# Performance work log

Hardware: AMD Instinct MI355X
Metric: run time of the kernel (lower is better)

Reference implementation:

```python
import jax, jax.numpy as jnp
import numpy as np

N_TIME = 512          # n_time_nodes
LATENT = 32           # latent_dim
HIDDEN = 64           # hidden_dim
N_MODES = 8           # r_fourier_modes
X_A0 = 0.3            # initial stoichiometry (anode)
CSANMAX = 28700.0     # max concentration scale
BASE_LOGIT = float(np.log(X_A0 / (1.0 - X_A0)))  # logit_from_fraction(x_a0)
FEAT_DIM = 1 + 2 * N_MODES   # [rho, cos(k*pi*rho), sin(k*pi*rho)]
IN_DIM = LATENT + FEAT_DIM
N_POINTS = 2_000_000


def setup_inputs() -> dict:
    key = jax.random.key(0)
    ks = jax.random.split(key, 8)
    time_idx = jax.random.randint(ks[0], (N_POINTS,), 0, N_TIME)
    rho = jax.random.uniform(ks[1], (N_POINTS,), dtype=jnp.float32)
    # trainable latent code per nonzero time node
    emb = jax.random.normal(ks[2], (N_TIME - 1, LATENT), dtype=jnp.float32) * 0.02
    # decoder_a: Linear(IN,HID)+SiLU, Linear(HID,HID)+SiLU, Linear(HID,1)
    W0 = jax.random.normal(ks[3], (IN_DIM, HIDDEN), dtype=jnp.float32) / np.sqrt(IN_DIM)
    b0 = jnp.zeros((HIDDEN,), jnp.float32)
    W1 = jax.random.normal(ks[4], (HIDDEN, HIDDEN), dtype=jnp.float32) / np.sqrt(HIDDEN)
    b1 = jnp.zeros((HIDDEN,), jnp.float32)
    Wout = jax.random.normal(ks[5], (HIDDEN, 1), dtype=jnp.float32) * 0.1
    bout = jnp.zeros((1,), jnp.float32)
    return {"time_idx": time_idx, "rho": rho, "emb": emb,
            "W0": W0, "b0": b0, "W1": W1, "b1": b1, "Wout": Wout, "bout": bout}


def _radius_features(rho):
    # [N] -> [N, 1 + 2*N_MODES]
    k = jnp.arange(1, N_MODES + 1, dtype=rho.dtype)
    ang = jnp.pi * rho[:, None] * k[None, :]
    return jnp.concatenate([rho[:, None], jnp.cos(ang), jnp.sin(ang)], axis=1)


def reference(time_idx, rho, emb, W0, b0, W1, b1, Wout, bout):
    # predicated version of the torch masked scatter: compute everywhere,
    # select initial-condition value where time_idx == 0
    idx = jnp.clip(time_idx - 1, 0, N_TIME - 2)       # safe gather index
    e = emb[idx]                                       # [N, LATENT]
    feat = _radius_features(rho)                       # [N, FEAT_DIM]
    h = jnp.concatenate([e, feat], axis=1)             # [N, IN_DIM]
    h = jax.nn.silu(h @ W0 + b0)
    h = jax.nn.silu(h @ W1 + b1)
    raw = (h @ Wout + bout)[:, 0]                      # [N]
    theta = jax.nn.sigmoid(raw + BASE_LOGIT)
    return jnp.where(time_idx == 0, X_A0 * CSANMAX, theta * CSANMAX)
```

## Files before the change

kernel.cpp:

```cpp
#include <hip/hip_runtime.h>
#include <stdint.h>


typedef _Float16 half8  __attribute__((ext_vector_type(8)));
typedef _Float16 half4v __attribute__((ext_vector_type(4)));
typedef _Float16 half2v __attribute__((ext_vector_type(2)));
typedef float f32x4 __attribute__((ext_vector_type(4)));

#define LOG2E 1.44269504088896340736f
#define BASE_LOGIT -0.84729786038720367f
#define CSANMAX 28700.0f
#define IC_VAL 8610.0f

__device__ __forceinline__ float fast_exp2(float x) { return __builtin_amdgcn_exp2f(x); }
__device__ __forceinline__ float fast_rcp(float x)  { return __builtin_amdgcn_rcpf(x); }
__device__ __forceinline__ float sigf(float x)  { return fast_rcp(1.0f + fast_exp2(-LOG2E * x)); }
__device__ __forceinline__ void silu2(float x0, float x1, float& y0, float& y1) {
  const float d0 = 1.0f + fast_exp2(-LOG2E * x0);
  const float d1 = 1.0f + fast_exp2(-LOG2E * x1);
  const float r  = fast_rcp(d0 * d1);
  y0 = x0 * d1 * r;
  y1 = x1 * d0 * r;
}
__device__ __forceinline__ half2v pkh(float a, float b) {
  return __builtin_bit_cast(half2v, __builtin_amdgcn_cvt_pkrtz(a, b));
}

union H8 { half8 v8; half2v v2[4]; };
union H4 { half4v v4; half2v v2[2]; };

template <int CTRL>
__device__ __forceinline__ float dpp_radd(float x) {
  int yi = __builtin_amdgcn_update_dpp(0, __builtin_bit_cast(int, x), CTRL, 0xF, 0xF, false);
  return x + __builtin_bit_cast(float, yi);
}
__device__ __forceinline__ float row_sum16(float x) {
  x = dpp_radd<0xB1>(x);
  x = dpp_radd<0x4E>(x);
  x = dpp_radd<0x141>(x);
  x = dpp_radd<0x140>(x);
  return x;
}

__global__ __launch_bounds__(128) void mlp_kernel(
    const int* __restrict__ tix, const float* __restrict__ rho,
    const float* __restrict__ emb, const float* __restrict__ W0,
    const float* __restrict__ b0, const float* __restrict__ W1,
    const float* __restrict__ b1, const float* __restrict__ Wout,
    const float* __restrict__ bout, float* __restrict__ out, int ngroups)
{
  __shared__ __align__(16) _Float16 ldsF[2][64][40];
  __shared__ __align__(16) _Float16 ldsH[2][2][16][72];

  const int tid  = threadIdx.x;
  const int wid  = tid >> 6;
  const int lane = tid & 63;
  const int m    = lane & 15;
  const int q    = lane >> 4;

  _Float16 (*F)[40]      = ldsF[wid];
  _Float16 (*Hd)[16][72] = ldsH[wid];

  half8 B0f[4][2], B1f[4][2];
#pragma unroll
  for (int t = 0; t < 4; ++t) {
#pragma unroll
    for (int s = 0; s < 2; ++s) {
      half8 f0, f1;
#pragma unroll
      for (int j = 0; j < 8; ++j) {
        const int k = s * 32 + q * 8 + j;
        const int n = t * 16 + m;
        const float v0 = (k < 49) ? W0[k * 64 + n] : ((k == 49) ? b0[n] : 0.0f);
        f0[j] = (_Float16)v0;
        f1[j] = (_Float16)W1[k * 64 + n];
      }
      B0f[t][s] = f0;
      B1f[t][s] = f1;
    }
  }
  float b1n[4], woutm[4];
#pragma unroll
  for (int t = 0; t < 4; ++t) {
    b1n[t]   = b1[t * 16 + m];
    woutm[t] = Wout[t * 16 + m];
  }
  const float boutBL = bout[0] + BASE_LOGIT;

  {
    half8 zc = (half8)(_Float16)0.0f;
    *(half8*)&F[lane][16] = zc;
    *(half8*)&F[lane][24] = zc;
  }

  const f32x4 z = {0.0f, 0.0f, 0.0f, 0.0f};
  const int gwaves = gridDim.x * 2;

  int g = blockIdx.x * 2 + wid;
  if (g >= ngroups) return;

  int   tiL = tix[g * 64 + lane];
  float rh  = rho[g * 64 + lane];

  for (; g < ngroups; g += gwaves) {
    const int gbase = g * 64;

    const int gn = (g + gwaves < ngroups) ? (g + gwaves) : g;
    const int   tiLn = tix[gn * 64 + lane];
    const float rhn  = rho[gn * 64 + lane];

    int tim4[4];
#pragma unroll
    for (int st = 0; st < 4; ++st) tim4[st] = __shfl(tiL, st * 16 + m, 64);
    const float* erow0 = emb + (size_t)min(max(tim4[0] - 1, 0), 510) * 32 + q * 8;
    f32x4 eA0 = *(const f32x4*)erow0;
    f32x4 eA1 = *(const f32x4*)(erow0 + 4);

    const float rev = 0.5f * rh;
    const float c1 = __builtin_amdgcn_cosf(rev);
    const float s1 = __builtin_amdgcn_sinf(rev);
    float cs[8], sn[8];
    cs[0] = c1; sn[0] = s1;
    {
      float cm2 = 1.0f, cm1 = c1, sm2 = 0.0f, sm1 = s1;
      const float tc = 2.0f * c1;
#pragma unroll
      for (int k = 1; k < 8; ++k) {
        const float ck = tc * cm1 - cm2;
        const float sk = tc * sm1 - sm2;
        cs[k] = ck; sn[k] = sk;
        cm2 = cm1; cm1 = ck; sm2 = sm1; sm1 = sk;
      }
    }
    H8 h0, h1;
    h0.v2[0] = pkh(rh,    cs[0]); h0.v2[1] = pkh(cs[1], cs[2]);
    h0.v2[2] = pkh(cs[3], cs[4]); h0.v2[3] = pkh(cs[5], cs[6]);
    h1.v2[0] = pkh(cs[7], sn[0]); h1.v2[1] = pkh(sn[1], sn[2]);
    h1.v2[2] = pkh(sn[3], sn[4]); h1.v2[3] = pkh(sn[5], sn[6]);
    *(half8*)&F[lane][0] = h0.v8;
    *(half8*)&F[lane][8] = h1.v8;
    *(half2v*)&F[lane][16] = pkh(sn[7], 1.0f);

    float dcar = 0.0f;

#pragma unroll
    for (int st = 0; st < 4; ++st) {
      _Float16 (*Hb)[72] = Hd[st & 1];

      f32x4 eB0, eB1;
      if (st < 3) {
        const float* erown = emb + (size_t)min(max(tim4[st + 1] - 1, 0), 510) * 32 + q * 8;
        eB0 = *(const f32x4*)erown;
        eB1 = *(const f32x4*)(erown + 4);
      }

      H8 X0;
      X0.v2[0] = pkh(eA0[0], eA0[1]); X0.v2[1] = pkh(eA0[2], eA0[3]);
      X0.v2[2] = pkh(eA1[0], eA1[1]); X0.v2[3] = pkh(eA1[2], eA1[3]);
      const half8 X1 = *(const half8*)&F[st * 16 + m][q * 8];

      f32x4 acc[4];
#pragma unroll
      for (int t = 0; t < 4; ++t) {
        f32x4 a = __builtin_amdgcn_mfma_f32_16x16x32_f16(B0f[t][0], X0.v8, z, 0, 0, 0);
        a = __builtin_amdgcn_mfma_f32_16x16x32_f16(B0f[t][1], X1, a, 0, 0, 0);
        acc[t] = a;
      }
#pragma unroll
      for (int t = 0; t < 4; ++t) {
        float s0, s1v, s2, s3;
        silu2(acc[t][0], acc[t][1], s0, s1v);
        silu2(acc[t][2], acc[t][3], s2, s3);
        H4 hh;
        hh.v2[0] = pkh(s0, s1v);
        hh.v2[1] = pkh(s2, s3);
        *(half4v*)&Hb[m][t * 16 + q * 4] = hh.v4;
      }

      const half8 Y0 = *(const half8*)&Hb[m][q * 8];
      const half8 Y1 = *(const half8*)&Hb[m][32 + q * 8];
#pragma unroll
      for (int t = 0; t < 4; ++t) {
        const f32x4 binit = {b1n[t], b1n[t], b1n[t], b1n[t]};
        f32x4 a = __builtin_amdgcn_mfma_f32_16x16x32_f16(Y0, B1f[t][0], binit, 0, 0, 0);
        a = __builtin_amdgcn_mfma_f32_16x16x32_f16(Y1, B1f[t][1], a, 0, 0, 0);
        acc[t] = a;
      }
      float dot0 = 0.0f, dot1 = 0.0f, dot2 = 0.0f, dot3 = 0.0f;
#pragma unroll
      for (int t = 0; t < 4; ++t) {
        float s0, s1v, s2, s3;
        silu2(acc[t][0], acc[t][1], s0, s1v);
        silu2(acc[t][2], acc[t][3], s2, s3);
        dot0 = fmaf(s0,  woutm[t], dot0);
        dot1 = fmaf(s1v, woutm[t], dot1);
        dot2 = fmaf(s2,  woutm[t], dot2);
        dot3 = fmaf(s3,  woutm[t], dot3);
      }
      dot0 = row_sum16(dot0);
      dot1 = row_sum16(dot1);
      dot2 = row_sum16(dot2);
      dot3 = row_sum16(dot3);
      const float dsel = (m & 2) ? ((m & 1) ? dot3 : dot2) : ((m & 1) ? dot1 : dot0);
      const float dg = __shfl(dsel, (m >> 2) * 16 + (m & 3), 64);
      dcar = (q == st) ? dg : dcar;

      eA0 = eB0; eA1 = eB1;
    }

    const float theta = sigf(dcar + boutBL);
    out[gbase + lane] = (tiL == 0) ? IC_VAL : theta * CSANMAX;

    tiL = tiLn; rh = rhn;
  }
}

extern "C" void kernel_launch(void* const* d_in, const int* in_sizes, int n_in,
                              void* d_out, int out_size, void* d_ws, size_t ws_size,
                              hipStream_t stream) {
  const int*   tix  = (const int*)d_in[0];
  const float* rho  = (const float*)d_in[1];
  const float* emb  = (const float*)d_in[2];
  const float* W0   = (const float*)d_in[3];
  const float* b0   = (const float*)d_in[4];
  const float* W1   = (const float*)d_in[5];
  const float* b1   = (const float*)d_in[6];
  const float* Wout = (const float*)d_in[7];
  const float* bout = (const float*)d_in[8];
  float* outp = (float*)d_out;

  const int n       = in_sizes[0];
  const int ngroups = n / 64;

  int grid = 2048;
  if (grid * 2 > ngroups) grid = (ngroups + 1) / 2;
  mlp_kernel<<<dim3(grid), dim3(128), 0, stream>>>(
      tix, rho, emb, W0, b0, W1, b1, Wout, bout, outp, ngroups);
}
```

Before: 178.9 us.

## Move MLP weights to shared LDS and compute Fourier features per MFMA stage

Weight fragments for both layers now live in LDS once per block of four waves and are read each stage, instead of sitting in 64 VGPRs per lane. The Fourier features are built directly in the MFMA operand layout for each 16-point sub-tile, with each lane quarter covering cos, sin, or rho/bias. The per-wave feature LDS buffer and the embedding prefetch are dropped, the W0 rows are reordered to match, and the block grows to 256 threads. The goal is lower register pressure and higher occupancy, paid for with extra LDS reads per stage, recomputed sin/cos, and no embedding prefetch.

Result: faster. 174.8 us (-2.3%).

```diff
diff --git a/kernel.cpp b/kernel.cpp
--- a/kernel.cpp
+++ b/kernel.cpp
@@ -42,15 +42,16 @@
   return x;
 }
 
-__global__ __launch_bounds__(128) void mlp_kernel(
+__global__ __launch_bounds__(256) void mlp_kernel(
     const int* __restrict__ tix, const float* __restrict__ rho,
     const float* __restrict__ emb, const float* __restrict__ W0,
     const float* __restrict__ b0, const float* __restrict__ W1,
     const float* __restrict__ b1, const float* __restrict__ Wout,
     const float* __restrict__ bout, float* __restrict__ out, int ngroups)
 {
-  __shared__ __align__(16) _Float16 ldsF[2][64][40];
-  __shared__ __align__(16) _Float16 ldsH[2][2][16][72];
+  __shared__ __align__(16) _Float16 Wlds0[2][4][64][8];
+  __shared__ __align__(16) _Float16 Wlds1[2][4][64][8];
+  __shared__ __align__(16) _Float16 ldsH[4][16][72];
 
   const int tid  = threadIdx.x;
   const int wid  = tid >> 6;
@@ -58,27 +59,36 @@
   const int m    = lane & 15;
   const int q    = lane >> 4;
 
-  _Float16 (*F)[40]      = ldsF[wid];
-  _Float16 (*Hd)[16][72] = ldsH[wid];
-
-  half8 B0f[4][2], B1f[4][2];
-#pragma unroll
-  for (int t = 0; t < 4; ++t) {
-#pragma unroll
-    for (int s = 0; s < 2; ++s) {
-      half8 f0, f1;
-#pragma unroll
-      for (int j = 0; j < 8; ++j) {
-        const int k = s * 32 + q * 8 + j;
-        const int n = t * 16 + m;
-        const float v0 = (k < 49) ? W0[k * 64 + n] : ((k == 49) ? b0[n] : 0.0f);
-        f0[j] = (_Float16)v0;
-        f1[j] = (_Float16)W1[k * 64 + n];
-      }
-      B0f[t][s] = f0;
-      B1f[t][s] = f1;
+  _Float16 (*Hb)[72] = ldsH[wid];
+
+  if (wid == 0) {
+#pragma unroll
+    for (int t = 0; t < 4; ++t) {
+#pragma unroll
+      for (int s = 0; s < 2; ++s) {
+        half8 f0, f1;
+#pragma unroll
+        for (int j = 0; j < 8; ++j) {
+          const int k = s * 32 + q * 8 + j;
+          const int n = t * 16 + m;
+          float v0;
+          if (k < 32) {
+            v0 = W0[k * 64 + n];
+          } else {
+            const int kn = k - 32;
+            v0 = (kn < 16) ? W0[(33 + kn) * 64 + n]
+               : (kn == 16) ? W0[32 * 64 + n]
+               : (kn == 17) ? b0[n] : 0.0f;
+          }
+          f0[j] = (_Float16)v0;
+          f1[j] = (_Float16)W1[k * 64 + n];
+        }
+        *(half8*)&Wlds0[s][t][lane][0] = f0;
+        *(half8*)&Wlds1[s][t][lane][0] = f1;
+      }
     }
   }
+
   float b1n[4], woutm[4];
 #pragma unroll
   for (int t = 0; t < 4; ++t) {
@@ -87,83 +97,73 @@
   }
   const float boutBL = bout[0] + BASE_LOGIT;
 
-  {
-    half8 zc = (half8)(_Float16)0.0f;
-    *(half8*)&F[lane][16] = zc;
-    *(half8*)&F[lane][24] = zc;
-  }
+  __syncthreads();
 
   const f32x4 z = {0.0f, 0.0f, 0.0f, 0.0f};
-  const int gwaves = gridDim.x * 2;
-
-  int g = blockIdx.x * 2 + wid;
+  const int gstride = gridDim.x * 4;
+
+  int g = blockIdx.x * 4 + wid;
   if (g >= ngroups) return;
 
   int   tiL = tix[g * 64 + lane];
   float rh  = rho[g * 64 + lane];
 
-  for (; g < ngroups; g += gwaves) {
+  for (; g < ngroups; g += gstride) {
     const int gbase = g * 64;
 
-    const int gn = (g + gwaves < ngroups) ? (g + gwaves) : g;
+    const int gn = (g + gstride < ngroups) ? (g + gstride) : g;
     const int   tiLn = tix[gn * 64 + lane];
     const float rhn  = rho[gn * 64 + lane];
 
-    int tim4[4];
-#pragma unroll
-    for (int st = 0; st < 4; ++st) tim4[st] = __shfl(tiL, st * 16 + m, 64);
-    const float* erow0 = emb + (size_t)min(max(tim4[0] - 1, 0), 510) * 32 + q * 8;
-    f32x4 eA0 = *(const f32x4*)erow0;
-    f32x4 eA1 = *(const f32x4*)(erow0 + 4);
-
-    const float rev = 0.5f * rh;
-    const float c1 = __builtin_amdgcn_cosf(rev);
-    const float s1 = __builtin_amdgcn_sinf(rev);
-    float cs[8], sn[8];
-    cs[0] = c1; sn[0] = s1;
-    {
-      float cm2 = 1.0f, cm1 = c1, sm2 = 0.0f, sm1 = s1;
-      const float tc = 2.0f * c1;
-#pragma unroll
-      for (int k = 1; k < 8; ++k) {
-        const float ck = tc * cm1 - cm2;
-        const float sk = tc * sm1 - sm2;
-        cs[k] = ck; sn[k] = sk;
-        cm2 = cm1; cm1 = ck; sm2 = sm1; sm1 = sk;
-      }
-    }
-    H8 h0, h1;
-    h0.v2[0] = pkh(rh,    cs[0]); h0.v2[1] = pkh(cs[1], cs[2]);
-    h0.v2[2] = pkh(cs[3], cs[4]); h0.v2[3] = pkh(cs[5], cs[6]);
-    h1.v2[0] = pkh(cs[7], sn[0]); h1.v2[1] = pkh(sn[1], sn[2]);
-    h1.v2[2] = pkh(sn[3], sn[4]); h1.v2[3] = pkh(sn[5], sn[6]);
-    *(half8*)&F[lane][0] = h0.v8;
-    *(half8*)&F[lane][8] = h1.v8;
-    *(half2v*)&F[lane][16] = pkh(sn[7], 1.0f);
-
     float dcar = 0.0f;
 
 #pragma unroll
     for (int st = 0; st < 4; ++st) {
-      _Float16 (*Hb)[72] = Hd[st & 1];
-
-      f32x4 eB0, eB1;
-      if (st < 3) {
-        const float* erown = emb + (size_t)min(max(tim4[st + 1] - 1, 0), 510) * 32 + q * 8;
-        eB0 = *(const f32x4*)erown;
-        eB1 = *(const f32x4*)(erown + 4);
-      }
-
+      const int tim  = __shfl(tiL, st * 16 + m, 64);
+      const int idxm = min(max(tim - 1, 0), 510);
+      const float* erow = emb + (size_t)idxm * 32 + q * 8;
+      const f32x4 e0 = *(const f32x4*)erow;
+      const f32x4 e1 = *(const f32x4*)(erow + 4);
+
+      const float rhp = __shfl(rh, st * 16 + m, 64);
+      const float rev = 0.5f * rhp;
+      const float c1  = __builtin_amdgcn_cosf(rev);
+      const float s1f = __builtin_amdgcn_sinf(rev);
+      const float tc  = 2.0f * c1;
+      const float x1v = (q == 0) ? c1 : s1f;
+      const float x0v = (q == 0) ? 1.0f : 0.0f;
+      const float x2v = tc * x1v - x0v;
+      const float x3v = tc * x2v - x1v;
+      const float x4v = tc * x3v - x2v;
+      const float x5v = tc * x4v - x3v;
+      const float x6v = tc * x5v - x4v;
+      const float x7v = tc * x6v - x5v;
+      const float x8v = tc * x7v - x6v;
+      H8 X1;
+      X1.v2[0] = pkh(x1v, x2v);
+      X1.v2[1] = pkh(x3v, x4v);
+      X1.v2[2] = pkh(x5v, x6v);
+      X1.v2[3] = pkh(x7v, x8v);
+      {
+        const half2v z2 = {};
+        const half2v pr = pkh(rhp, 1.0f);
+        const bool hi = (q >= 2);
+        X1.v2[0] = hi ? ((q == 2) ? pr : z2) : X1.v2[0];
+        X1.v2[1] = hi ? z2 : X1.v2[1];
+        X1.v2[2] = hi ? z2 : X1.v2[2];
+        X1.v2[3] = hi ? z2 : X1.v2[3];
+      }
       H8 X0;
-      X0.v2[0] = pkh(eA0[0], eA0[1]); X0.v2[1] = pkh(eA0[2], eA0[3]);
-      X0.v2[2] = pkh(eA1[0], eA1[1]); X0.v2[3] = pkh(eA1[2], eA1[3]);
-      const half8 X1 = *(const half8*)&F[st * 16 + m][q * 8];
+      X0.v2[0] = pkh(e0[0], e0[1]); X0.v2[1] = pkh(e0[2], e0[3]);
+      X0.v2[2] = pkh(e1[0], e1[1]); X0.v2[3] = pkh(e1[2], e1[3]);
 
       f32x4 acc[4];
 #pragma unroll
       for (int t = 0; t < 4; ++t) {
-        f32x4 a = __builtin_amdgcn_mfma_f32_16x16x32_f16(B0f[t][0], X0.v8, z, 0, 0, 0);
-        a = __builtin_amdgcn_mfma_f32_16x16x32_f16(B0f[t][1], X1, a, 0, 0, 0);
+        const half8 wA = *(const half8*)&Wlds0[0][t][lane][0];
+        const half8 wB = *(const half8*)&Wlds0[1][t][lane][0];
+        f32x4 a = __builtin_amdgcn_mfma_f32_16x16x32_f16(wA, X0.v8, z, 0, 0, 0);
+        a = __builtin_amdgcn_mfma_f32_16x16x32_f16(wB, X1.v8, a, 0, 0, 0);
         acc[t] = a;
       }
 #pragma unroll
@@ -181,9 +181,11 @@
       const half8 Y1 = *(const half8*)&Hb[m][32 + q * 8];
 #pragma unroll
       for (int t = 0; t < 4; ++t) {
+        const half8 w1A = *(const half8*)&Wlds1[0][t][lane][0];
+        const half8 w1B = *(const half8*)&Wlds1[1][t][lane][0];
         const f32x4 binit = {b1n[t], b1n[t], b1n[t], b1n[t]};
-        f32x4 a = __builtin_amdgcn_mfma_f32_16x16x32_f16(Y0, B1f[t][0], binit, 0, 0, 0);
-        a = __builtin_amdgcn_mfma_f32_16x16x32_f16(Y1, B1f[t][1], a, 0, 0, 0);
+        f32x4 a = __builtin_amdgcn_mfma_f32_16x16x32_f16(Y0, w1A, binit, 0, 0, 0);
+        a = __builtin_amdgcn_mfma_f32_16x16x32_f16(Y1, w1B, a, 0, 0, 0);
         acc[t] = a;
       }
       float dot0 = 0.0f, dot1 = 0.0f, dot2 = 0.0f, dot3 = 0.0f;
@@ -204,8 +206,6 @@
       const float dsel = (m & 2) ? ((m & 1) ? dot3 : dot2) : ((m & 1) ? dot1 : dot0);
       const float dg = __shfl(dsel, (m >> 2) * 16 + (m & 3), 64);
       dcar = (q == st) ? dg : dcar;
-
-      eA0 = eB0; eA1 = eB1;
     }
 
     const float theta = sigf(dcar + boutBL);
@@ -232,8 +232,9 @@
   const int n       = in_sizes[0];
   const int ngroups = n / 64;
 
-  int grid = 2048;
-  if (grid * 2 > ngroups) grid = (ngroups + 1) / 2;
-  mlp_kernel<<<dim3(grid), dim3(128), 0, stream>>>(
+  int grid = 1536;
+  const int maxg = (ngroups + 3) / 4;
+  if (grid > maxg) grid = maxg;
+  mlp_kernel<<<dim3(grid), dim3(256), 0, stream>>>(
       tix, rho, emb, W0, b0, W1, b1, Wout, bout, outp, ngroups);
 }
```
